# Kernel optimization log

Measured on AMD Instinct MI355X. Metric: run time of the kernel, lower is better.

## Reference

```python
import jax, jax.numpy as jnp
import numpy as np

E = 96   # embed dim (MultiheadAttention(96, 6))
H = 6    # heads
DH = E // H  # head dim = 16


def setup_inputs() -> dict:
    key = jax.random.key(0)
    ks = jax.random.split(key, 6)
    N, G = 4096, 64
    feats = jax.random.normal(ks[0], (N, E), jnp.float32)
    group = jax.random.randint(ks[1], (N,), 0, G)
    s = 1.0 / np.sqrt(E)
    # nn.MultiheadAttention packed in_proj [3E, E] and out_proj [E, E]
    w_in = jax.random.uniform(ks[2], (3 * E, E), jnp.float32, -s, s)
    b_in = jnp.zeros((3 * E,), jnp.float32)
    w_out = jax.random.uniform(ks[3], (E, E), jnp.float32, -s, s)
    b_out = jnp.zeros((E,), jnp.float32)
    # classifier Linear(96, 1)
    w_cls = jax.random.uniform(ks[4], (1, E), jnp.float32, -s, s)
    b_cls = jnp.zeros((1,), jnp.float32)
    return {"feats": feats, "group": group, "w_in": w_in, "b_in": b_in,
            "w_out": w_out, "b_out": b_out, "w_cls": w_cls, "b_cls": b_cls}


def reference(feats, group, w_in, b_in, w_out, b_out, w_cls, b_cls):
    # Per-group self-attention: softmax restricted to rows of the same group
    # is mathematically identical to running MHA on each group separately.
    N = feats.shape[0]
    qkv = feats @ w_in.T + b_in                     # [N, 3E]
    q, k, v = jnp.split(qkv, 3, axis=-1)            # each [N, E]
    to_heads = lambda t: t.reshape(N, H, DH).transpose(1, 0, 2)  # [H, N, DH]
    q = to_heads(q) * (1.0 / np.sqrt(DH))
    k = to_heads(k)
    v = to_heads(v)
    scores = jnp.einsum('hnd,hmd->hnm', q, k)       # [H, N, N]
    same_group = group[:, None] == group[None, :]   # [N, N] (diag always True)
    scores = jnp.where(same_group[None], scores, jnp.float32(-1e9))
    attn = jax.nn.softmax(scores, axis=-1)
    out = jnp.einsum('hnm,hmd->hnd', attn, v)       # [H, N, DH]
    out = out.transpose(1, 0, 2).reshape(N, E)
    out = out @ w_out.T + b_out                     # out_proj
    logits = out @ w_cls.T + b_cls                  # [N, 1]
    return jax.nn.sigmoid(logits)[:, 0]             # cluster_scores [N]
```

## Files before the change

### kernel.cpp

```cpp
#include <hip/hip_runtime.h>
#include <math.h>

#define N 4096
#define E 96
#define H 6
#define DH 16
#define G 64
#define CMAX 128
#define KSTR 19
#define NW 8
#define NT 512

__global__ __launch_bounds__(NT) void fused_kernel(const float* __restrict__ feats,
                                                   const int* __restrict__ grp,
                                                   const float* __restrict__ w_in,
                                                   const float* __restrict__ b_in,
                                                   const float* __restrict__ w_out,
                                                   const float* __restrict__ w_cls,
                                                   float* __restrict__ logit) {
    __shared__ float wl[48 * 100];
    __shared__ float qh[CMAX * KSTR];
    __shared__ float kh[CMAX * KSTR];
    __shared__ float vh[CMAX * KSTR];
    __shared__ float ps[NW * CMAX];
    __shared__ int   bucket[CMAX];
    __shared__ float wfh[DH];
    __shared__ int   scnt;

    int g = blockIdx.x & 63;
    int h = blockIdx.x >> 6;
    int tid = threadIdx.x, lane = tid & 63, wv = tid >> 6;

    if (tid == 0) scnt = 0;
    __syncthreads();

    int gv[8];
    #pragma unroll
    for (int c8 = 0; c8 < 8; ++c8)
        gv[c8] = grp[((wv + NW * c8) << 6) + lane];
    #pragma unroll
    for (int c8 = 0; c8 < 8; ++c8) {
        int i = ((wv + NW * c8) << 6) + lane;
        bool mt = (gv[c8] == g);
        unsigned long long mask = __ballot(mt);
        int base = 0;
        if (lane == 0) base = atomicAdd(&scnt, __popcll(mask));
        base = __shfl(base, 0, 64);
        if (mt) {
            int pos = base + __popcll(mask & ((1ULL << lane) - 1ULL));
            if (pos < CMAX) bucket[pos] = i;
        }
    }

    for (int idx = tid; idx < 48 * 24; idx += NT) {
        int ci = idx / 24, j = idx % 24;
        int part = ci >> 4, dd = ci & 15;
        int gcol = part * E + h * DH + dd;
        *(float4*)(wl + ci * 100 + j * 4) = *(const float4*)(w_in + gcol * E + j * 4);
    }

    if (wv == 0) {
        int dd = lane & 15, u4 = lane >> 4;
        float s = 0.f;
        for (int u = u4 * 24; u < u4 * 24 + 24; ++u)
            s += w_cls[u] * w_out[u * E + h * DH + dd];
        s += __shfl_xor(s, 16, 64);
        s += __shfl_xor(s, 32, 64);
        if (lane < DH) wfh[lane] = s;
    }
    __syncthreads();

    int cnt = scnt; if (cnt > CMAX) cnt = CMAX;
    if (cnt == 0) return;

    int d = tid & 15, rr = tid >> 4;
    float bq = b_in[h * DH + d];
    float bk = b_in[E + h * DH + d];
    float bv = b_in[2 * E + h * DH + d];
    const float4* wq  = (const float4*)(wl + d * 100);
    const float4* wk  = (const float4*)(wl + (16 + d) * 100);
    const float4* wvp = (const float4*)(wl + (32 + d) * 100);
    for (int rbase = 0; rbase < cnt; rbase += 32) {
        int r = rbase + rr;
        if (r < cnt) {
            const float4* fp = (const float4*)(feats + bucket[r] * E);
            float sq = 0.f, sk = 0.f, sv = 0.f;
            #pragma unroll
            for (int e4 = 0; e4 < 24; ++e4) {
                float4 f = fp[e4];
                float4 a = wq[e4], b = wk[e4], c = wvp[e4];
                sq += f.x*a.x + f.y*a.y + f.z*a.z + f.w*a.w;
                sk += f.x*b.x + f.y*b.y + f.z*b.z + f.w*b.w;
                sv += f.x*c.x + f.y*c.y + f.z*c.z + f.w*c.w;
            }
            qh[r * KSTR + d] = (sq + bq) * 0.25f;
            kh[r * KSTR + d] = sk + bk;
            vh[r * KSTR + d] = sv + bv;
        }
    }
    __syncthreads();

    for (int r = wv; r < cnt; r += NW) {
        float qv[16];
        #pragma unroll
        for (int e = 0; e < 16; ++e) qv[e] = qh[r * KSTR + e];

        float a0 = 0.f;
        #pragma unroll
        for (int e = 0; e < 16; ++e) a0 += qv[e] * kh[lane * KSTR + e];
        float s0 = (lane < cnt) ? a0 : -INFINITY;
        float s1 = -INFINITY;
        if (cnt > 64) {
            float a1 = 0.f;
            #pragma unroll
            for (int e = 0; e < 16; ++e) a1 += qv[e] * kh[(64 + lane) * KSTR + e];
            s1 = (64 + lane < cnt) ? a1 : -INFINITY;
        }

        float m = fmaxf(s0, s1);
        #pragma unroll
        for (int o = 32; o >= 1; o >>= 1) m = fmaxf(m, __shfl_xor(m, o, 64));
        float p0 = __expf(s0 - m);
        float p1 = (cnt > 64) ? __expf(s1 - m) : 0.f;
        float l = p0 + p1;
        #pragma unroll
        for (int o = 32; o >= 1; o >>= 1) l += __shfl_xor(l, o, 64);
        ps[wv * CMAX + lane] = p0;
        ps[wv * CMAX + 64 + lane] = p1;

        int mm4 = lane >> 4, dd = lane & 15;
        float acc = 0.f;
        for (int m2 = mm4; m2 < cnt; m2 += 4)
            acc += ps[wv * CMAX + m2] * vh[m2 * KSTR + dd];
        acc += __shfl_xor(acc, 16, 64);
        acc += __shfl_xor(acc, 32, 64);

        float part = (acc / l) * wfh[dd];
        part += __shfl_xor(part, 1, 64);
        part += __shfl_xor(part, 2, 64);
        part += __shfl_xor(part, 4, 64);
        part += __shfl_xor(part, 8, 64);
        if (lane == 0) atomicAdd(&logit[bucket[r]], part);
    }
}

__global__ __launch_bounds__(1024) void sigmoid_kernel(const float* __restrict__ logit,
                                                       const float* __restrict__ w_cls,
                                                       const float* __restrict__ b_out,
                                                       const float* __restrict__ b_cls,
                                                       float* __restrict__ out) {
    __shared__ float sbias;
    int tid = threadIdx.x;
    if (tid < 64) {
        float s = w_cls[tid] * b_out[tid];
        if (tid < 32) s += w_cls[tid + 64] * b_out[tid + 64];
        #pragma unroll
        for (int o = 32; o >= 1; o >>= 1) s += __shfl_xor(s, o, 64);
        if (tid == 0) sbias = s + b_cls[0];
    }
    __syncthreads();
    int i = blockIdx.x * 1024 + tid;
    out[i] = 1.f / (1.f + __expf(-(logit[i] + sbias)));
}

extern "C" void kernel_launch(void* const* d_in, const int* in_sizes, int n_in,
                              void* d_out, int out_size, void* d_ws, size_t ws_size,
                              hipStream_t stream) {
    const float* feats = (const float*)d_in[0];
    const int*   grp   = (const int*)  d_in[1];
    const float* w_in  = (const float*)d_in[2];
    const float* b_in  = (const float*)d_in[3];
    const float* w_out = (const float*)d_in[4];
    const float* b_out = (const float*)d_in[5];
    const float* w_cls = (const float*)d_in[6];
    const float* b_cls = (const float*)d_in[7];
    float* out = (float*)d_out;

    float* logit = (float*)d_ws;

    hipMemsetAsync(logit, 0, N * sizeof(float), stream);
    fused_kernel<<<G * H, NT, 0, stream>>>(feats, grp, w_in, b_in, w_out, w_cls, logit);
    sigmoid_kernel<<<N / 1024, 1024, 0, stream>>>(logit, w_cls, b_out, b_cls, out);
}
```

Before: 108.6 us.

## Split query rows across two blocks per group-head and drop atomics and memset

Doubles the grid so each (group, head) pair is handled by two blocks, each computing queries and attention for alternating rows while both recompute the full K/V. Per-head partial logits are written to a [N,8] buffer instead of being atomically accumulated, so the memset is removed and the sigmoid kernel sums the six partials. The bucket build becomes deterministic via per-chunk ballot masks and a prefix scan, and the PV loop is unrolled with zero-padded V. This trades duplicated K/V projection work for more parallelism and fewer launches.

```diff
diff --git a/kernel.cpp b/kernel.cpp
--- a/kernel.cpp
+++ b/kernel.cpp
@@ -11,55 +11,47 @@
 #define NW 8
 #define NT 512
 
-__global__ __launch_bounds__(NT) void fused_kernel(const float* __restrict__ feats,
-                                                   const int* __restrict__ grp,
-                                                   const float* __restrict__ w_in,
-                                                   const float* __restrict__ b_in,
-                                                   const float* __restrict__ w_out,
-                                                   const float* __restrict__ w_cls,
-                                                   float* __restrict__ logit) {
+__global__ __launch_bounds__(NT, 6) void fused_kernel(const float* __restrict__ feats,
+                                                      const int* __restrict__ grp,
+                                                      const float* __restrict__ w_in,
+                                                      const float* __restrict__ b_in,
+                                                      const float* __restrict__ w_out,
+                                                      const float* __restrict__ w_cls,
+                                                      float* __restrict__ part) {
     __shared__ float wl[48 * 100];
-    __shared__ float qh[CMAX * KSTR];
     __shared__ float kh[CMAX * KSTR];
     __shared__ float vh[CMAX * KSTR];
+    __shared__ float qh[64 * KSTR];
     __shared__ float ps[NW * CMAX];
     __shared__ int   bucket[CMAX];
+    __shared__ unsigned long long smask[64];
+    __shared__ int   scount[64];
+    __shared__ int   soffs[64];
     __shared__ float wfh[DH];
     __shared__ int   scnt;
 
-    int g = blockIdx.x & 63;
-    int h = blockIdx.x >> 6;
+    int g  = blockIdx.x & 63;
+    int hh = blockIdx.x >> 6;
+    int h  = hh >> 1;
+    int hb = hh & 1;
     int tid = threadIdx.x, lane = tid & 63, wv = tid >> 6;
 
-    if (tid == 0) scnt = 0;
-    __syncthreads();
-
-    int gv[8];
-    #pragma unroll
-    for (int c8 = 0; c8 < 8; ++c8)
-        gv[c8] = grp[((wv + NW * c8) << 6) + lane];
     #pragma unroll
     for (int c8 = 0; c8 < 8; ++c8) {
-        int i = ((wv + NW * c8) << 6) + lane;
-        bool mt = (gv[c8] == g);
+        int cc = wv * 8 + c8;
+        bool mt = (grp[(cc << 6) + lane] == g);
         unsigned long long mask = __ballot(mt);
-        int base = 0;
-        if (lane == 0) base = atomicAdd(&scnt, __popcll(mask));
-        base = __shfl(base, 0, 64);
-        if (mt) {
-            int pos = base + __popcll(mask & ((1ULL << lane) - 1ULL));
-            if (pos < CMAX) bucket[pos] = i;
-        }
+        if (lane == 0) { smask[cc] = mask; scount[cc] = __popcll(mask); }
     }
 
     for (int idx = tid; idx < 48 * 24; idx += NT) {
         int ci = idx / 24, j = idx % 24;
-        int part = ci >> 4, dd = ci & 15;
-        int gcol = part * E + h * DH + dd;
+        int pp = ci >> 4, dd = ci & 15;
+        int gcol = pp * E + h * DH + dd;
         *(float4*)(wl + ci * 100 + j * 4) = *(const float4*)(w_in + gcol * E + j * 4);
     }
 
-    if (wv == 0) {
+    if (wv == 7) {
         int dd = lane & 15, u4 = lane >> 4;
         float s = 0.f;
         for (int u = u4 * 24; u < u4 * 24 + 24; ++u)
@@ -70,40 +62,82 @@
     }
     __syncthreads();
 
+    if (wv == 0) {
+        int v = scount[lane];
+        int x = v;
+        #pragma unroll
+        for (int o = 1; o < 64; o <<= 1) {
+            int y = __shfl_up(x, o, 64);
+            if (lane >= o) x += y;
+        }
+        soffs[lane] = x - v;
+        if (lane == 63) scnt = x;
+    } else {
+        for (int idx = tid - 64; idx < CMAX * KSTR; idx += NT - 64) vh[idx] = 0.f;
+    }
+    __syncthreads();
+
     int cnt = scnt; if (cnt > CMAX) cnt = CMAX;
-    if (cnt == 0) return;
+
+    #pragma unroll
+    for (int c8 = 0; c8 < 8; ++c8) {
+        int cc = wv * 8 + c8;
+        unsigned long long mask = smask[cc];
+        if ((mask >> lane) & 1ULL) {
+            int pos = soffs[cc] + __popcll(mask & ((1ULL << lane) - 1ULL));
+            if (pos < CMAX) bucket[pos] = (cc << 6) + lane;
+        }
+    }
+    __syncthreads();
 
     int d = tid & 15, rr = tid >> 4;
-    float bq = b_in[h * DH + d];
     float bk = b_in[E + h * DH + d];
     float bv = b_in[2 * E + h * DH + d];
-    const float4* wq  = (const float4*)(wl + d * 100);
     const float4* wk  = (const float4*)(wl + (16 + d) * 100);
     const float4* wvp = (const float4*)(wl + (32 + d) * 100);
-    for (int rbase = 0; rbase < cnt; rbase += 32) {
-        int r = rbase + rr;
-        if (r < cnt) {
-            const float4* fp = (const float4*)(feats + bucket[r] * E);
-            float sq = 0.f, sk = 0.f, sv = 0.f;
+    #pragma unroll
+    for (int p = 0; p < 4; ++p) {
+        int s = rr + 32 * p;
+        if (s < cnt) {
+            const float4* fp = (const float4*)(feats + bucket[s] * E);
+            float sk = 0.f, sv = 0.f;
             #pragma unroll
             for (int e4 = 0; e4 < 24; ++e4) {
                 float4 f = fp[e4];
-                float4 a = wq[e4], b = wk[e4], c = wvp[e4];
-                sq += f.x*a.x + f.y*a.y + f.z*a.z + f.w*a.w;
+                float4 b = wk[e4], c = wvp[e4];
                 sk += f.x*b.x + f.y*b.y + f.z*b.z + f.w*b.w;
                 sv += f.x*c.x + f.y*c.y + f.z*c.z + f.w*c.w;
             }
-            qh[r * KSTR + d] = (sq + bq) * 0.25f;
-            kh[r * KSTR + d] = sk + bk;
-            vh[r * KSTR + d] = sv + bv;
-        }
-    }
-    __syncthreads();
-
-    for (int r = wv; r < cnt; r += NW) {
+            kh[s * KSTR + d] = sk + bk;
+            vh[s * KSTR + d] = sv + bv;
+        }
+    }
+
+    float bq = b_in[h * DH + d];
+    const float4* wq = (const float4*)(wl + d * 100);
+    #pragma unroll
+    for (int p = 0; p < 2; ++p) {
+        int j = rr + 32 * p;
+        int r = 2 * j + hb;
+        if (r < cnt) {
+            const float4* fp = (const float4*)(feats + bucket[r] * E);
+            float sq = 0.f;
+            #pragma unroll
+            for (int e4 = 0; e4 < 24; ++e4) {
+                float4 f = fp[e4];
+                float4 a = wq[e4];
+                sq += f.x*a.x + f.y*a.y + f.z*a.z + f.w*a.w;
+            }
+            qh[j * KSTR + d] = (sq + bq) * 0.25f;
+        }
+    }
+    __syncthreads();
+
+    for (int j = wv; 2 * j + hb < cnt; j += NW) {
+        int r = 2 * j + hb;
         float qv[16];
         #pragma unroll
-        for (int e = 0; e < 16; ++e) qv[e] = qh[r * KSTR + e];
+        for (int e = 0; e < 16; ++e) qv[e] = qh[j * KSTR + e];
 
         float a0 = 0.f;
         #pragma unroll
@@ -130,25 +164,35 @@
 
         int mm4 = lane >> 4, dd = lane & 15;
         float acc = 0.f;
-        for (int m2 = mm4; m2 < cnt; m2 += 4)
+        #pragma unroll
+        for (int k = 0; k < 16; ++k) {
+            int m2 = mm4 + 4 * k;
             acc += ps[wv * CMAX + m2] * vh[m2 * KSTR + dd];
+        }
+        if (cnt > 64) {
+            #pragma unroll
+            for (int k = 16; k < 32; ++k) {
+                int m2 = mm4 + 4 * k;
+                acc += ps[wv * CMAX + m2] * vh[m2 * KSTR + dd];
+            }
+        }
         acc += __shfl_xor(acc, 16, 64);
         acc += __shfl_xor(acc, 32, 64);
 
-        float part = (acc / l) * wfh[dd];
-        part += __shfl_xor(part, 1, 64);
-        part += __shfl_xor(part, 2, 64);
-        part += __shfl_xor(part, 4, 64);
-        part += __shfl_xor(part, 8, 64);
-        if (lane == 0) atomicAdd(&logit[bucket[r]], part);
+        float pt = (acc / l) * wfh[dd];
+        pt += __shfl_xor(pt, 1, 64);
+        pt += __shfl_xor(pt, 2, 64);
+        pt += __shfl_xor(pt, 4, 64);
+        pt += __shfl_xor(pt, 8, 64);
+        if (lane == 0) part[bucket[r] * 8 + h] = pt;
     }
 }
 
-__global__ __launch_bounds__(1024) void sigmoid_kernel(const float* __restrict__ logit,
-                                                       const float* __restrict__ w_cls,
-                                                       const float* __restrict__ b_out,
-                                                       const float* __restrict__ b_cls,
-                                                       float* __restrict__ out) {
+__global__ __launch_bounds__(512) void sigmoid_kernel(const float* __restrict__ part,
+                                                      const float* __restrict__ w_cls,
+                                                      const float* __restrict__ b_out,
+                                                      const float* __restrict__ b_cls,
+                                                      float* __restrict__ out) {
     __shared__ float sbias;
     int tid = threadIdx.x;
     if (tid < 64) {
@@ -159,8 +203,11 @@
         if (tid == 0) sbias = s + b_cls[0];
     }
     __syncthreads();
-    int i = blockIdx.x * 1024 + tid;
-    out[i] = 1.f / (1.f + __expf(-(logit[i] + sbias)));
+    int i = blockIdx.x * 512 + tid;
+    const float4* p = (const float4*)(part + i * 8);
+    float4 u = p[0], v = p[1];
+    float s = u.x + u.y + u.z + u.w + v.x + v.y + sbias;
+    out[i] = 1.f / (1.f + __expf(-s));
 }
 
 extern "C" void kernel_launch(void* const* d_in, const int* in_sizes, int n_in,
@@ -176,9 +223,8 @@
     const float* b_cls = (const float*)d_in[7];
     float* out = (float*)d_out;
 
-    float* logit = (float*)d_ws;
-
-    hipMemsetAsync(logit, 0, N * sizeof(float), stream);
-    fused_kernel<<<G * H, NT, 0, stream>>>(feats, grp, w_in, b_in, w_out, w_cls, logit);
-    sigmoid_kernel<<<N / 1024, 1024, 0, stream>>>(logit, w_cls, b_out, b_cls, out);
+    float* part = (float*)d_ws;
+
+    fused_kernel<<<G * H * 2, NT, 0, stream>>>(feats, grp, w_in, b_in, w_out, w_cls, part);
+    sigmoid_kernel<<<N / 512, 512, 0, stream>>>(part, w_cls, b_out, b_cls, out);
 }
```

Measured after the change: 110.4 us. No clear change (+1.7%).
